# Optimization experiments

Hardware: AMD Instinct MI355X
Metric: run time of the kernel (lower is better)

## Reference

```python
import jax, jax.numpy as jnp
import numpy as np

BN_EPS = 1e-5


def _conv(x, w):
    # x: [N, Cin, H, W], w: [Cout, Cin, kh, kw], stride 1, padding 1 (same for 3x3)
    return jax.lax.conv_general_dilated(
        x, w, window_strides=(1, 1), padding=[(1, 1), (1, 1)],
        dimension_numbers=('NCHW', 'OIHW', 'NCHW'))


def setup_inputs() -> dict:
    key = jax.random.key(0)
    ks = jax.random.split(key, 4)
    T, N, Cin, Cout, H, W = 16, 4, 64, 64, 64, 64
    x = jax.random.normal(ks[0], (T, N, Cin, H, W), dtype=jnp.float32)
    # conv_x2h: Conv2d(Cin, 4*Cout, k=3, s=1, p=1, bias=True) + BatchNorm2d(4*Cout)
    Wx = jax.random.normal(ks[1], (4 * Cout, Cin, 3, 3), dtype=jnp.float32) * 0.05
    bx = jax.random.normal(ks[2], (4 * Cout,), dtype=jnp.float32) * 0.05
    gamma = jnp.ones((4 * Cout,), dtype=jnp.float32)
    beta = jnp.zeros((4 * Cout,), dtype=jnp.float32)
    # conv_h2h: Conv2d(Cout, 4*Cout, k=3, p=1, bias=False)
    Wh = jax.random.normal(ks[3], (4 * Cout, Cout, 3, 3), dtype=jnp.float32) * 0.05
    return {"x": x, "Wx": Wx, "bx": bx, "gamma": gamma, "beta": beta, "Wh": Wh}


def reference(x, Wx, bx, gamma, beta, Wh):
    T, N, Cin, H, W = x.shape
    hidden = Wh.shape[1]

    # ---- SequenceWise(Conv2d + BatchNorm(train) + Identity) ----
    xf = x.reshape(T * N, Cin, H, W)
    y = _conv(xf, Wx) + bx[None, :, None, None]
    mean = jnp.mean(y, axis=(0, 2, 3))
    var = jnp.var(y, axis=(0, 2, 3))  # biased, as torch BN uses for normalization
    y = (y - mean[None, :, None, None]) * jax.lax.rsqrt(var[None, :, None, None] + BN_EPS)
    y = y * gamma[None, :, None, None] + beta[None, :, None, None]
    y = y.reshape(T, N, 4 * hidden, H, W)

    # ---- ConvLSTMCell recurrence over time ----
    # zeros init is exactly equivalent to prev_h/prev_c = None:
    # conv_h2h(0) = 0 (no bias) and f*0 + i*g = i*g.
    h0 = jnp.zeros((N, hidden, H, W), dtype=x.dtype)
    c0 = jnp.zeros((N, hidden, H, W), dtype=x.dtype)

    def step(carry, xt):
        h, c = carry
        tmp = _conv(h, Wh) + xt
        cc_i, cc_f, cc_o, cc_g = jnp.split(tmp, 4, axis=1)
        i = jax.nn.sigmoid(cc_i)
        f = jax.nn.sigmoid(cc_f)
        o = jax.nn.sigmoid(cc_o)
        g = jnp.tanh(cc_g)
        c = f * c + i * g
        h = o * jnp.tanh(c)
        return (h, c), h

    _, hs = jax.lax.scan(step, (h0, c0), y)
    return hs  # [T, N, hidden, H, W]
```

## Files before the change

kernel.cpp:

```cpp
#include <hip/hip_runtime.h>
#include <hip/hip_bf16.h>

typedef float        f32x4  __attribute__((ext_vector_type(4)));
typedef unsigned int u32x4  __attribute__((ext_vector_type(4)));
typedef __bf16       bf16x8 __attribute__((ext_vector_type(8)));

__device__ __forceinline__ unsigned short f2bf(float f) {
    unsigned u = __builtin_bit_cast(unsigned, f);
    u += 0x7fffu + ((u >> 16) & 1u);
    return (unsigned short)(u >> 16);
}
__device__ __forceinline__ float bf2f(unsigned short u) {
    union { unsigned ui; float f; } c; c.ui = ((unsigned)u) << 16; return c.f;
}
__device__ __forceinline__ void gload_lds16(const void* g, void* l) {
    __builtin_amdgcn_global_load_lds(
        (const __attribute__((address_space(1))) unsigned int*)g,
        (__attribute__((address_space(3))) unsigned int*)l, 16, 0, 0);
}

__global__ __launch_bounds__(256) void k_xT(const float* __restrict__ x,
                                            unsigned short* __restrict__ xT) {
    int bid = blockIdx.x;
    int img = bid >> 4;
    int p   = (bid & 15) * 256 + threadIdx.x;
    const float* xi = x + (size_t)img * 64 * 4096 + p;
    unsigned short r[64];
#pragma unroll
    for (int ci = 0; ci < 64; ++ci) r[ci] = f2bf(xi[(size_t)ci * 4096]);
    u32x4* dst = (u32x4*)(xT + ((size_t)img * 4096 + p) * 64);
#pragma unroll
    for (int c8 = 0; c8 < 8; ++c8) dst[c8] = *(u32x4*)&r[c8 * 8];
}

__global__ __launch_bounds__(256) void k_pack(const float* __restrict__ W,
                                              unsigned short* __restrict__ Ap) {
    int idx = blockIdx.x * 256 + threadIdx.x;
    if (idx >= 256 * 576) return;
    int row = idx / 576, k = idx % 576;
    int tap = k / 64, cil = k % 64;
    int kb = cil >> 5, w32 = cil & 31;
    int s = w32 >> 3, e = w32 & 7;
    int ci = kb * 32 + ((s ^ (row & 3)) << 3) + e;
    int co = (row & 3) * 64 + (row >> 2);
    Ap[idx] = f2bf(W[((size_t)co * 64 + ci) * 9 + tap]);
}

__global__ __launch_bounds__(256) void k_conv0(
    const unsigned short* __restrict__ src,
    const unsigned short* __restrict__ Ap,
    unsigned short* __restrict__ ybf,
    float2* __restrict__ prt)
{
    constexpr int TH = 16, N_ = 4, HR = 18;

    __shared__ __align__(16) unsigned short halo[HR * 18 * 64];
    __shared__ __align__(16) unsigned short As[2][2048];

    const int bid  = blockIdx.x;
    const int xcd  = bid & 7;
    const int sidx = bid >> 3;
    const int grp  = sidx & 3;
    const int pairG = (sidx >> 2) * 8 + xcd;
    const int tile = pairG & 15;
    const int img  = pairG >> 4;
    const int py0 = (tile >> 2) * TH, px0 = (tile & 3) * 16;
    const int tid = threadIdx.x;
    const int wv = tid >> 6, lane = tid & 63;
    const int cl = lane & 15, q = lane >> 4;
    const int rowbase = grp * 64;

    f32x4 acc[4][N_];
#pragma unroll
    for (int m = 0; m < 4; ++m)
#pragma unroll
        for (int n = 0; n < N_; ++n)
            acc[m][n] = (f32x4){0.f, 0.f, 0.f, 0.f};

    {
        const char* agp = (const char*)Ap +
            (size_t)(rowbase + (tid >> 2)) * 1152 + (tid & 3) * 16;
        char* AsL = (char*)&As[0][0] + tid * 16;
        gload_lds16(agp, AsL);

        const unsigned short* sb = src + (size_t)img * 4096 * 64;
        char* hB = (char*)halo;
        for (int tau = tid; tau < HR * 144; tau += 256) {
            int s = tau & 7, hcc = (tau >> 3) % 18, hrr = tau / 144;
            int gy = py0 + hrr - 1, gx = px0 + hcc - 1;
            u32x4 v = {0u, 0u, 0u, 0u};
            if ((unsigned)gy < 64u && (unsigned)gx < 64u)
                v = *(const u32x4*)(sb + ((gy * 64 + gx) * 64 + s * 8));
            *(u32x4*)(hB + (hrr * 18 + hcc) * 128 + ((s * 16) ^ ((hcc & 7) << 4))) = v;
        }
        __syncthreads();

        int aoff[4];
#pragma unroll
        for (int m = 0; m < 4; ++m)
            aoff[m] = (m * 16 + cl) * 64 + ((q * 16) ^ ((cl & 3) << 4));

        const char* AsRd = (const char*)&As[0][0];
#pragma unroll
        for (int ks = 0; ks < 18; ++ks) {
            const int buf = ks & 1;
            if (ks < 17)
                gload_lds16(agp + (ks + 1) * 64, (char*)&As[buf ^ 1][0] + tid * 16);

            const int tap = ks >> 1, kb = ks & 1;
            const int ky = tap / 3, kx = tap - ky * 3;

            u32x4 af[4];
#pragma unroll
            for (int m = 0; m < 4; ++m)
                af[m] = *(const u32x4*)(AsRd + buf * 4096 + aoff[m]);

            int hcv  = cl + kx;
            int cbase = hcv * 128 + ((kb * 64 + q * 16) ^ ((hcv & 7) << 4));
#pragma unroll
            for (int n = 0; n < N_; ++n) {
                int hr = wv * N_ + n + ky;
                u32x4 bv = *(const u32x4*)(hB + hr * 2304 + cbase);
                bf16x8 bfr = __builtin_bit_cast(bf16x8, bv);
#pragma unroll
                for (int m = 0; m < 4; ++m)
                    acc[m][n] = __builtin_amdgcn_mfma_f32_16x16x32_bf16(
                        __builtin_bit_cast(bf16x8, af[m]), bfr, acc[m][n], 0, 0, 0);
            }
            __syncthreads();
        }
    }

#pragma unroll
    for (int m = 0; m < 4; ++m) {
#pragma unroll
        for (int n = 0; n < N_; ++n) {
            int pix = (py0 + wv * N_ + n) * 64 + px0 + cl;
            uint2 w;
            w.x = (unsigned)f2bf(acc[m][n][0]) | ((unsigned)f2bf(acc[m][n][1]) << 16);
            w.y = (unsigned)f2bf(acc[m][n][2]) | ((unsigned)f2bf(acc[m][n][3]) << 16);
            *(uint2*)(ybf + ((size_t)img * 4096 + pix) * 256 + rowbase + m * 16 + q * 4) = w;
        }
    }
    float* bnred = (float*)halo;
#pragma unroll
    for (int m = 0; m < 4; ++m) {
#pragma unroll
        for (int j = 0; j < 4; ++j) {
            float s = 0.f, qq = 0.f;
#pragma unroll
            for (int n = 0; n < N_; ++n) {
                float v = acc[m][n][j];
                s += v; qq += v * v;
            }
#pragma unroll
            for (int mask = 1; mask <= 8; mask <<= 1) {
                s  += __shfl_xor(s,  mask, 64);
                qq += __shfl_xor(qq, mask, 64);
            }
            if (cl == 0) {
                int ci_ = (wv * 4 + q) * 16 + m * 4 + j;
                bnred[ci_ * 2]     = s;
                bnred[ci_ * 2 + 1] = qq;
            }
        }
    }
    __syncthreads();
    if (tid < 64) {
        int m_ = tid >> 4, qj = tid & 15;
        float s = 0.f, qq = 0.f;
#pragma unroll
        for (int w = 0; w < 4; ++w) {
            int idx = ((w * 4 + (qj >> 2)) * 16 + m_ * 4 + (qj & 3)) * 2;
            s += bnred[idx]; qq += bnred[idx + 1];
        }
        prt[(size_t)(rowbase + tid) * 1024 + img * 16 + tile] = make_float2(s, qq);
    }
}

__global__ __launch_bounds__(256) void k_bn_fin(
    const float2* __restrict__ prt, const float* __restrict__ bx,
    const float* __restrict__ gamma, const float* __restrict__ beta,
    float* __restrict__ ss) {
    int c = blockIdx.x;
    const float2* p = prt + (size_t)c * 1024;
    float s = 0.f, sq = 0.f;
    for (int i = threadIdx.x; i < 1024; i += 256) {
        float2 v = p[i]; s += v.x; sq += v.y;
    }
    __shared__ float rs[256], rq[256];
    int tid = threadIdx.x;
    rs[tid] = s; rq[tid] = sq;
    __syncthreads();
    for (int off = 128; off > 0; off >>= 1) {
        if (tid < off) { rs[tid] += rs[tid + off]; rq[tid] += rq[tid + off]; }
        __syncthreads();
    }
    if (tid == 0) {
        int co = (c & 3) * 64 + (c >> 2);
        float mean = rs[0] * (1.f / 262144.f);
        float var  = rq[0] * (1.f / 262144.f) - mean * mean;
        float sc   = gamma[co] * rsqrtf(var + 1e-5f);
        ss[c]       = sc;
        ss[256 + c] = beta[co] - mean * sc;
        (void)bx;
    }
}

__global__ __launch_bounds__(256) void k_step(
    const unsigned short* __restrict__ hin,
    const unsigned short* __restrict__ Ap,
    const unsigned short* __restrict__ ybf,
    const float* __restrict__ ss,
    float* __restrict__ cst,
    unsigned short* __restrict__ hout,
    float* __restrict__ out,
    int t, int first)
{
    constexpr int TH = 8, N_ = 2, HR = 10;

    __shared__ __align__(16) unsigned short halo[HR * 18 * 64];
    __shared__ __align__(16) unsigned short As[2][2048];

    const int bid  = blockIdx.x;
    const int xcd  = bid & 7;
    const int sidx = bid >> 3;
    const int grp  = sidx & 3;
    const int pairG = (sidx >> 2) * 8 + xcd;
    const int tile = pairG & 31;
    const int img  = pairG >> 5;
    const int py0 = (tile >> 2) * TH, px0 = (tile & 3) * 16;
    const int tid = threadIdx.x;
    const int wv = tid >> 6, lane = tid & 63;
    const int cl = lane & 15, q = lane >> 4;
    const int rowbase = grp * 64;

    uint2 ypre[4][N_];
    float cpre[4][N_];
#pragma unroll
    for (int m = 0; m < 4; ++m) {
        int hc = grp * 16 + m * 4 + q;
#pragma unroll
        for (int n = 0; n < N_; ++n) {
            int pix = (py0 + wv * N_ + n) * 64 + px0 + cl;
            ypre[m][n] = *(const uint2*)(ybf +
                ((size_t)(t * 4 + img) * 4096 + pix) * 256 + hc * 4);
            cpre[m][n] = cst[((size_t)img * 64 + hc) * 4096 + pix];
        }
    }

    f32x4 acc[4][N_];
#pragma unroll
    for (int m = 0; m < 4; ++m)
#pragma unroll
        for (int n = 0; n < N_; ++n)
            acc[m][n] = (f32x4){0.f, 0.f, 0.f, 0.f};

    if (!first) {
        const char* agp = (const char*)Ap +
            (size_t)(rowbase + (tid >> 2)) * 1152 + (tid & 3) * 16;
        gload_lds16(agp, (char*)&As[0][0] + tid * 16);

        const unsigned short* sb = hin + (size_t)img * 4096 * 64;
        char* hB = (char*)halo;
        for (int tau = tid; tau < HR * 144; tau += 256) {
            int s = tau & 7, hcc = (tau >> 3) % 18, hrr = tau / 144;
            int gy = py0 + hrr - 1, gx = px0 + hcc - 1;
            u32x4 v = {0u, 0u, 0u, 0u};
            if ((unsigned)gy < 64u && (unsigned)gx < 64u)
                v = *(const u32x4*)(sb + ((gy * 64 + gx) * 64 + s * 8));
            *(u32x4*)(hB + (hrr * 18 + hcc) * 128 + ((s * 16) ^ ((hcc & 7) << 4))) = v;
        }
        __syncthreads();

        int aoff[4];
#pragma unroll
        for (int m = 0; m < 4; ++m)
            aoff[m] = (m * 16 + cl) * 64 + ((q * 16) ^ ((cl & 3) << 4));

        const char* AsRd = (const char*)&As[0][0];
#pragma unroll
        for (int ks = 0; ks < 18; ++ks) {
            const int buf = ks & 1;
            if (ks < 17)
                gload_lds16(agp + (ks + 1) * 64, (char*)&As[buf ^ 1][0] + tid * 16);

            const int tap = ks >> 1, kb = ks & 1;
            const int ky = tap / 3, kx = tap - ky * 3;

            u32x4 af[4];
#pragma unroll
            for (int m = 0; m < 4; ++m)
                af[m] = *(const u32x4*)(AsRd + buf * 4096 + aoff[m]);

            int hcv  = cl + kx;
            int cbase = hcv * 128 + ((kb * 64 + q * 16) ^ ((hcv & 7) << 4));
#pragma unroll
            for (int n = 0; n < N_; ++n) {
                int hr = wv * N_ + n + ky;
                u32x4 bv = *(const u32x4*)(hB + hr * 2304 + cbase);
                bf16x8 bfr = __builtin_bit_cast(bf16x8, bv);
#pragma unroll
                for (int m = 0; m < 4; ++m)
                    acc[m][n] = __builtin_amdgcn_mfma_f32_16x16x32_bf16(
                        __builtin_bit_cast(bf16x8, af[m]), bfr, acc[m][n], 0, 0, 0);
            }
            __syncthreads();
        }
    }

    unsigned short* hbounce = halo;
    const f32x4* sc4 = (const f32x4*)ss;
    const f32x4* sh4 = (const f32x4*)(ss + 256);
#pragma unroll
    for (int m = 0; m < 4; ++m) {
        int hc = grp * 16 + m * 4 + q;
        f32x4 sc = sc4[hc], sh = sh4[hc];
#pragma unroll
        for (int n = 0; n < N_; ++n) {
            int pix = (py0 + wv * N_ + n) * 64 + px0 + cl;
            uint2 yv = ypre[m][n];
            float tmp[4];
            tmp[0] = acc[m][n][0] + sc[0] * bf2f((unsigned short)(yv.x & 0xffffu)) + sh[0];
            tmp[1] = acc[m][n][1] + sc[1] * bf2f((unsigned short)(yv.x >> 16))     + sh[1];
            tmp[2] = acc[m][n][2] + sc[2] * bf2f((unsigned short)(yv.y & 0xffffu)) + sh[2];
            tmp[3] = acc[m][n][3] + sc[3] * bf2f((unsigned short)(yv.y >> 16))     + sh[3];
            float iv = 1.f / (1.f + __expf(-tmp[0]));
            float fv = 1.f / (1.f + __expf(-tmp[1]));
            float ov = 1.f / (1.f + __expf(-tmp[2]));
            float e2 = __expf(2.f * tmp[3]);
            float gv = 1.f - 2.f / (e2 + 1.f);
            size_t cidx = ((size_t)img * 64 + hc) * 4096 + pix;
            float cnew = fv * cpre[m][n] + iv * gv;
            cst[cidx] = cnew;
            float e2c = __expf(2.f * cnew);
            float hv  = ov * (1.f - 2.f / (e2c + 1.f));
            out[((size_t)(t * 4 + img) * 64 + hc) * 4096 + pix] = hv;
            hbounce[((wv * N_ + n) * 16 + cl) * 16 + m * 4 + q] = f2bf(hv);
        }
    }
    __syncthreads();
    if (tid < TH * 16) {
        int pixg = (py0 + (tid >> 4)) * 64 + px0 + (tid & 15);
        u32x4* dst = (u32x4*)(hout + ((size_t)img * 4096 + pixg) * 64 + grp * 16);
        u32x4* s0  = (u32x4*)(hbounce + tid * 16);
        dst[0] = s0[0];
        dst[1] = s0[1];
    }
}

extern "C" void kernel_launch(void* const* d_in, const int* in_sizes, int n_in,
                              void* d_out, int out_size, void* d_ws, size_t ws_size,
                              hipStream_t stream) {
    const float* x     = (const float*)d_in[0];
    const float* Wx    = (const float*)d_in[1];
    const float* bx    = (const float*)d_in[2];
    const float* gamma = (const float*)d_in[3];
    const float* beta  = (const float*)d_in[4];
    const float* Wh    = (const float*)d_in[5];
    float* out = (float*)d_out;

    char* ws = (char*)d_ws;
    unsigned short* y   = (unsigned short*)ws;
    unsigned short* Axp = (unsigned short*)(ws + 134217728);
    unsigned short* Ahp = (unsigned short*)(ws + 134512640);
    float*          ss  = (float*)(ws + 134807552);
    float*          cs  = (float*)(ws + 134809600);
    float2*         prt = (float2*)(ws + 139003904);
    unsigned short* hA  = (unsigned short*)(ws + 139003904);
    unsigned short* hB  = (unsigned short*)(ws + 141101056);

    unsigned short* xT = (unsigned short*)d_out;

    k_xT  <<<1024, 256, 0, stream>>>(x, xT);
    k_pack<<< 576, 256, 0, stream>>>(Wx, Axp);
    k_pack<<< 576, 256, 0, stream>>>(Wh, Ahp);
    hipMemsetAsync(cs, 0, 4194304, stream);

    k_conv0<<<4096, 256, 0, stream>>>(xT, Axp, y, prt);
    k_bn_fin<<<256, 256, 0, stream>>>(prt, bx, gamma, beta, ss);

    unsigned short* hbuf[2] = {hA, hB};
    for (int t = 0; t < 16; ++t) {
        k_step<<<512, 256, 0, stream>>>(hbuf[t & 1], Ahp, y, ss, cs,
                                        hbuf[(t + 1) & 1], out, t, t == 0 ? 1 : 0);
    }
}
```

Before: 389.8 us.

## Halve conv0 halo LDS by staging channel halves, reorder K loop, transpose via LDS

The packed weight K order changes from tap-major to channel-half-major, so conv0 stages only 32 input channels of the halo at a time, halving halo LDS. This allows a launch bound of 5 blocks per SM for more occupancy, at the cost of an extra restaging barrier mid-loop. k_xT now transposes through swizzled shared memory so global stores are coalesced 16-byte writes. The cell-state memset is removed by treating the first step's c as zero in k_step.

```diff
diff --git a/kernel.cpp b/kernel.cpp
--- a/kernel.cpp
+++ b/kernel.cpp
@@ -21,16 +21,30 @@
 
 __global__ __launch_bounds__(256) void k_xT(const float* __restrict__ x,
                                             unsigned short* __restrict__ xT) {
-    int bid = blockIdx.x;
-    int img = bid >> 4;
-    int p   = (bid & 15) * 256 + threadIdx.x;
-    const float* xi = x + (size_t)img * 64 * 4096 + p;
-    unsigned short r[64];
-#pragma unroll
-    for (int ci = 0; ci < 64; ++ci) r[ci] = f2bf(xi[(size_t)ci * 4096]);
-    u32x4* dst = (u32x4*)(xT + ((size_t)img * 4096 + p) * 64);
-#pragma unroll
-    for (int c8 = 0; c8 < 8; ++c8) dst[c8] = *(u32x4*)&r[c8 * 8];
+    __shared__ unsigned int tl[256 * 32];
+    const int img = blockIdx.x >> 4;
+    const int p0  = (blockIdx.x & 15) * 256;
+    const int tid = threadIdx.x;
+    const float* xi = x + (size_t)img * 64 * 4096 + p0 + tid;
+#pragma unroll
+    for (int cp = 0; cp < 32; ++cp) {
+        float a = xi[(size_t)(2 * cp) * 4096];
+        float b = xi[(size_t)(2 * cp + 1) * 4096];
+        unsigned v = (unsigned)f2bf(a) | ((unsigned)f2bf(b) << 16);
+        tl[tid * 32 + (cp ^ (tid & 31))] = v;
+    }
+    __syncthreads();
+    unsigned short* dst = xT + ((size_t)img * 4096 + p0) * 64;
+#pragma unroll
+    for (int k = 0; k < 8; ++k) {
+        int c = tid + k * 256;
+        int pix = c >> 3, slot = c & 7;
+        unsigned w[4];
+#pragma unroll
+        for (int i = 0; i < 4; ++i)
+            w[i] = tl[pix * 32 + ((slot * 4 + i) ^ (pix & 31))];
+        *(u32x4*)(dst + (size_t)pix * 64 + slot * 8) = *(u32x4*)w;
+    }
 }
 
 __global__ __launch_bounds__(256) void k_pack(const float* __restrict__ W,
@@ -38,15 +52,15 @@
     int idx = blockIdx.x * 256 + threadIdx.x;
     if (idx >= 256 * 576) return;
     int row = idx / 576, k = idx % 576;
-    int tap = k / 64, cil = k % 64;
-    int kb = cil >> 5, w32 = cil & 31;
+    int kb = k / 288, r2 = k % 288;
+    int tap = r2 / 32, w32 = r2 % 32;
     int s = w32 >> 3, e = w32 & 7;
     int ci = kb * 32 + ((s ^ (row & 3)) << 3) + e;
     int co = (row & 3) * 64 + (row >> 2);
     Ap[idx] = f2bf(W[((size_t)co * 64 + ci) * 9 + tap]);
 }
 
-__global__ __launch_bounds__(256) void k_conv0(
+__global__ __launch_bounds__(256, 5) void k_conv0(
     const unsigned short* __restrict__ src,
     const unsigned short* __restrict__ Ap,
     unsigned short* __restrict__ ybf,
@@ -54,7 +68,7 @@
 {
     constexpr int TH = 16, N_ = 4, HR = 18;
 
-    __shared__ __align__(16) unsigned short halo[HR * 18 * 64];
+    __shared__ __align__(16) unsigned short halo[HR * 18 * 32];
     __shared__ __align__(16) unsigned short As[2][2048];
 
     const int bid  = blockIdx.x;
@@ -78,21 +92,24 @@
             acc[m][n] = (f32x4){0.f, 0.f, 0.f, 0.f};
 
     {
+        const unsigned short* sb = src + (size_t)img * 4096 * 64;
+        char* hB = (char*)halo;
+        auto stage_halo = [&](int kb) {
+            for (int tau = tid; tau < HR * 18 * 4; tau += 256) {
+                int s = tau & 3, pos = tau >> 2;
+                int hcc = pos % 18, hrr = pos / 18;
+                int gy = py0 + hrr - 1, gx = px0 + hcc - 1;
+                u32x4 v = {0u, 0u, 0u, 0u};
+                if ((unsigned)gy < 64u && (unsigned)gx < 64u)
+                    v = *(const u32x4*)(sb + ((gy * 64 + gx) * 64 + kb * 32 + s * 8));
+                *(u32x4*)(hB + pos * 64 + ((s ^ (hcc & 3)) << 4)) = v;
+            }
+        };
+
         const char* agp = (const char*)Ap +
             (size_t)(rowbase + (tid >> 2)) * 1152 + (tid & 3) * 16;
-        char* AsL = (char*)&As[0][0] + tid * 16;
-        gload_lds16(agp, AsL);
-
-        const unsigned short* sb = src + (size_t)img * 4096 * 64;
-        char* hB = (char*)halo;
-        for (int tau = tid; tau < HR * 144; tau += 256) {
-            int s = tau & 7, hcc = (tau >> 3) % 18, hrr = tau / 144;
-            int gy = py0 + hrr - 1, gx = px0 + hcc - 1;
-            u32x4 v = {0u, 0u, 0u, 0u};
-            if ((unsigned)gy < 64u && (unsigned)gx < 64u)
-                v = *(const u32x4*)(sb + ((gy * 64 + gx) * 64 + s * 8));
-            *(u32x4*)(hB + (hrr * 18 + hcc) * 128 + ((s * 16) ^ ((hcc & 7) << 4))) = v;
-        }
+        gload_lds16(agp, (char*)&As[0][0] + tid * 16);
+        stage_halo(0);
         __syncthreads();
 
         int aoff[4];
@@ -107,7 +124,7 @@
             if (ks < 17)
                 gload_lds16(agp + (ks + 1) * 64, (char*)&As[buf ^ 1][0] + tid * 16);
 
-            const int tap = ks >> 1, kb = ks & 1;
+            const int tap = ks % 9;
             const int ky = tap / 3, kx = tap - ky * 3;
 
             u32x4 af[4];
@@ -116,16 +133,20 @@
                 af[m] = *(const u32x4*)(AsRd + buf * 4096 + aoff[m]);
 
             int hcv  = cl + kx;
-            int cbase = hcv * 128 + ((kb * 64 + q * 16) ^ ((hcv & 7) << 4));
+            int poff = (q ^ (hcv & 3)) << 4;
 #pragma unroll
             for (int n = 0; n < N_; ++n) {
-                int hr = wv * N_ + n + ky;
-                u32x4 bv = *(const u32x4*)(hB + hr * 2304 + cbase);
+                int pos = (wv * N_ + n + ky) * 18 + hcv;
+                u32x4 bv = *(const u32x4*)(hB + pos * 64 + poff);
                 bf16x8 bfr = __builtin_bit_cast(bf16x8, bv);
 #pragma unroll
                 for (int m = 0; m < 4; ++m)
                     acc[m][n] = __builtin_amdgcn_mfma_f32_16x16x32_bf16(
                         __builtin_bit_cast(bf16x8, af[m]), bfr, acc[m][n], 0, 0, 0);
+            }
+            if (ks == 8) {
+                __syncthreads();
+                stage_halo(1);
             }
             __syncthreads();
         }
@@ -245,7 +266,7 @@
             int pix = (py0 + wv * N_ + n) * 64 + px0 + cl;
             ypre[m][n] = *(const uint2*)(ybf +
                 ((size_t)(t * 4 + img) * 4096 + pix) * 256 + hc * 4);
-            cpre[m][n] = cst[((size_t)img * 64 + hc) * 4096 + pix];
+            cpre[m][n] = first ? 0.f : cst[((size_t)img * 64 + hc) * 4096 + pix];
         }
     }
 
@@ -285,7 +306,7 @@
             if (ks < 17)
                 gload_lds16(agp + (ks + 1) * 64, (char*)&As[buf ^ 1][0] + tid * 16);
 
-            const int tap = ks >> 1, kb = ks & 1;
+            const int kb = ks / 9, tap = ks % 9;
             const int ky = tap / 3, kx = tap - ky * 3;
 
             u32x4 af[4];
@@ -375,7 +396,6 @@
     k_xT  <<<1024, 256, 0, stream>>>(x, xT);
     k_pack<<< 576, 256, 0, stream>>>(Wx, Axp);
     k_pack<<< 576, 256, 0, stream>>>(Wh, Ahp);
-    hipMemsetAsync(cs, 0, 4194304, stream);
 
     k_conv0<<<4096, 256, 0, stream>>>(xT, Axp, y, prt);
     k_bn_fin<<<256, 256, 0, stream>>>(prt, bx, gamma, beta, ss);
```

Measured after the change: 608.5 us. 56.1% more time.
